# Kernel tuning notes

Hardware: AMD Instinct MI355X
Metric: run time of the kernel (lower is better)

Reference implementation:

```python
import jax, jax.numpy as jnp
import numpy as np
from jax import lax

KERNEL_SIZE = 5
BOUNDARY_WIDTH = 10


def setup_inputs() -> dict:
    key = jax.random.key(0)
    x_in = jax.random.normal(key, (4, 16, 720, 1440), dtype=jnp.float32)
    return {"x_in": x_in}


def _box_sum(a, k):
    """Sum over a k x k window on the last two dims, zero-padded (SAME).
    Zero padding + mask-count division reproduces the clipped-window average."""
    window = (1,) * (a.ndim - 2) + (k, k)
    strides = (1,) * a.ndim
    return lax.reduce_window(a, jnp.array(0, a.dtype), lax.add, window, strides, "SAME")


def reference(x_in) -> jnp.ndarray:
    k = KERNEL_SIZE
    bw = BOUNDARY_WIDTH
    H, W = x_in.shape[-2], x_in.shape[-1]

    ii = jnp.arange(H)
    jj = jnp.arange(W)
    # boundary mask [H, W]: True within boundary_width of any edge
    mb = (((ii < bw) | (ii >= H - bw))[:, None]
          | ((jj < bw) | (jj >= W - bw))[None, :])
    mb_f = mb.astype(x_in.dtype)
    mi_f = 1.0 - mb_f

    # windowed sums of same-class neighbors (zero padding = clipped window)
    num_b = _box_sum(x_in * mb_f, k)   # contributions from boundary pixels
    num_i = _box_sum(x_in * mi_f, k)   # contributions from interior pixels
    cnt_b = _box_sum(mb_f, k)          # [H, W] counts, broadcast over leading dims
    cnt_i = _box_sum(mi_f, k)

    num = jnp.where(mb, num_b, num_i)
    cnt = jnp.where(mb, cnt_b, cnt_i)  # >= 1 wherever selected (pixel counts itself)
    return num / cnt
```

## Files before the change

kernel.cpp:

```cpp
#include <hip/hip_runtime.h>


#define HH 720
#define WW 1440
#define PLANE (HH * WW)
#define NPLANES 64


#define NG 354
#define NCHUNK 29
#define CHUNK 24

__device__ __forceinline__ float4 hsum5(const float* __restrict__ p) {
    const float2 l = *(const float2*)(p - 2);
    const float4 m = *(const float4*)(p);
    const float2 r = *(const float2*)(p + 4);
    float4 h;
    h.x = l.x + l.y + m.x + m.y + m.z;
    h.y = h.x - l.x + m.w;
    h.z = h.y - l.y + r.x;
    h.w = h.z - m.x + r.y;
    return h;
}

__global__ __launch_bounds__(256) void fast_kernel(const float* __restrict__ x,
                                                   float* __restrict__ out) {
    const int id = blockIdx.x * 256 + threadIdx.x;
    if (id >= NG * NCHUNK) return;
    const int chunk = id / NG;
    const int g     = id - chunk * NG;
    const int j0    = 12 + 4 * g;
    const int row0  = 12 + chunk * CHUNK;

    const float* __restrict__ xp = x + (size_t)blockIdx.y * PLANE;
    float* __restrict__ op       = out + (size_t)blockIdx.y * PLANE;

    float4 h[5];
#pragma unroll
    for (int t = 0; t < 4; ++t) {
        h[t] = hsum5(xp + (row0 - 2 + t) * WW + j0);
    }

#pragma unroll
    for (int t = 0; t < CHUNK; ++t) {
        const int r = row0 + t;
        h[(t + 4) % 5] = hsum5(xp + (r + 2) * WW + j0);
        float4 v;
        v.x = ((h[0].x + h[1].x) + (h[2].x + h[3].x)) + h[4].x;
        v.y = ((h[0].y + h[1].y) + (h[2].y + h[3].y)) + h[4].y;
        v.z = ((h[0].z + h[1].z) + (h[2].z + h[3].z)) + h[4].z;
        v.w = ((h[0].w + h[1].w) + (h[2].w + h[3].w)) + h[4].w;
        const float s = 1.0f / 25.0f;
        v.x *= s; v.y *= s; v.z *= s; v.w *= s;
        *(float4*)(op + r * WW + j0) = v;
    }
}


#define NEDGE 51264

__global__ __launch_bounds__(256) void edge_kernel(const float* __restrict__ x,
                                                   float* __restrict__ out) {
    const int p = blockIdx.x * 256 + threadIdx.x;
    if (p >= NEDGE) return;
    int i, j;
    if (p < 34560) {
        i = p / 1440;
        j = p - i * 1440;
        if (i >= 12) i += 696;
    } else {
        const int q  = p - 34560;
        const int qi = q / 24;
        const int r  = q - qi * 24;
        i = 12 + qi;
        j = (r < 12) ? r : r + 1416;
    }

    const float* __restrict__ xp = x + (size_t)blockIdx.y * PLANE;
    const bool cb = (i < 10) | (i >= 710) | (j < 10) | (j >= 1430);

    float s = 0.0f, cnt = 0.0f;
#pragma unroll
    for (int di = -2; di <= 2; ++di) {
#pragma unroll
        for (int dj = -2; dj <= 2; ++dj) {
            const int ni = i + di, nj = j + dj;
            const bool inb = ((unsigned)ni < (unsigned)HH) & ((unsigned)nj < (unsigned)WW);
            const bool nb  = (ni < 10) | (ni >= 710) | (nj < 10) | (nj >= 1430);
            const int ci = min(max(ni, 0), HH - 1);
            const int cj = min(max(nj, 0), WW - 1);
            const float v = xp[ci * WW + cj];
            const float w = (inb && (nb == cb)) ? 1.0f : 0.0f;
            s += w * v;
            cnt += w;
        }
    }
    out[(size_t)blockIdx.y * PLANE + i * WW + j] = s / cnt;
}

extern "C" void kernel_launch(void* const* d_in, const int* in_sizes, int n_in,
                              void* d_out, int out_size, void* d_ws, size_t ws_size,
                              hipStream_t stream) {
    const float* x = (const float*)d_in[0];
    float* out = (float*)d_out;

    dim3 gf((NG * NCHUNK + 255) / 256, NPLANES);
    hipLaunchKernelGGL(fast_kernel, gf, dim3(256), 0, stream, x, out);

    dim3 ge((NEDGE + 255) / 256, NPLANES);
    hipLaunchKernelGGL(edge_kernel, ge, dim3(256), 0, stream, x, out);
}
```

Measured before the change: 469.3 us.

## Prefetch next row in rotating-register stencil loop and shrink row chunks

Splits each row's load from its horizontal sum so the next row's raw values are loaded one iteration ahead of use. The fully unrolled 24-row loop becomes a non-unrolled loop over a five-row register rotation, which cuts code size and register pressure. Chunks drop from 24 to 20 rows with more chunks, giving more threads. A bounds guard skips rows past 707, at the cost of some redundant work and an added branch in the last chunk.

```diff
diff --git a/kernel.cpp b/kernel.cpp
--- a/kernel.cpp
+++ b/kernel.cpp
@@ -6,21 +6,42 @@
 #define PLANE (HH * WW)
 #define NPLANES 64
 
+#define NG 354
+#define CHUNK 20
+#define NCHUNK 35
 
-#define NG 354
-#define NCHUNK 29
-#define CHUNK 24
+struct Raw { float2 l; float4 m; float2 r; };
 
-__device__ __forceinline__ float4 hsum5(const float* __restrict__ p) {
-    const float2 l = *(const float2*)(p - 2);
-    const float4 m = *(const float4*)(p);
-    const float2 r = *(const float2*)(p + 4);
+__device__ __forceinline__ Raw load_row(const float* __restrict__ p) {
+    Raw o;
+    o.l = *(const float2*)(p - 2);
+    o.m = *(const float4*)(p);
+    o.r = *(const float2*)(p + 4);
+    return o;
+}
+
+__device__ __forceinline__ float4 combine(const Raw& w) {
     float4 h;
-    h.x = l.x + l.y + m.x + m.y + m.z;
-    h.y = h.x - l.x + m.w;
-    h.z = h.y - l.y + r.x;
-    h.w = h.z - m.x + r.y;
+    h.x = w.l.x + w.l.y + w.m.x + w.m.y + w.m.z;
+    h.y = h.x - w.l.x + w.m.w;
+    h.z = h.y - w.l.y + w.r.x;
+    h.w = h.z - w.m.x + w.r.y;
     return h;
+}
+
+__device__ __forceinline__ void emit(const float4& a, const float4& b,
+                                     const float4& c, const float4& d,
+                                     const float4& e, float* __restrict__ q,
+                                     int r) {
+    if (r < 708) {
+        const float s = 1.0f / 25.0f;
+        float4 v;
+        v.x = (((a.x + b.x) + (c.x + d.x)) + e.x) * s;
+        v.y = (((a.y + b.y) + (c.y + d.y)) + e.y) * s;
+        v.z = (((a.z + b.z) + (c.z + d.z)) + e.z) * s;
+        v.w = (((a.w + b.w) + (c.w + d.w)) + e.w) * s;
+        *(float4*)q = v;
+    }
 }
 
 __global__ __launch_bounds__(256) void fast_kernel(const float* __restrict__ x,
@@ -35,24 +56,29 @@
     const float* __restrict__ xp = x + (size_t)blockIdx.y * PLANE;
     float* __restrict__ op       = out + (size_t)blockIdx.y * PLANE;
 
-    float4 h[5];
-#pragma unroll
-    for (int t = 0; t < 4; ++t) {
-        h[t] = hsum5(xp + (row0 - 2 + t) * WW + j0);
-    }
+    const float* p = xp + (row0 - 2) * WW + j0;
+    float4 h0 = combine(load_row(p)); p += WW;
+    float4 h1 = combine(load_row(p)); p += WW;
+    float4 h2 = combine(load_row(p)); p += WW;
+    float4 h3 = combine(load_row(p)); p += WW;
+    float4 h4;
+    Raw pre = load_row(p); p += WW;
 
-#pragma unroll
-    for (int t = 0; t < CHUNK; ++t) {
-        const int r = row0 + t;
-        h[(t + 4) % 5] = hsum5(xp + (r + 2) * WW + j0);
-        float4 v;
-        v.x = ((h[0].x + h[1].x) + (h[2].x + h[3].x)) + h[4].x;
-        v.y = ((h[0].y + h[1].y) + (h[2].y + h[3].y)) + h[4].y;
-        v.z = ((h[0].z + h[1].z) + (h[2].z + h[3].z)) + h[4].z;
-        v.w = ((h[0].w + h[1].w) + (h[2].w + h[3].w)) + h[4].w;
-        const float s = 1.0f / 25.0f;
-        v.x *= s; v.y *= s; v.z *= s; v.w *= s;
-        *(float4*)(op + r * WW + j0) = v;
+    float* q = op + row0 * WW + j0;
+    int r = row0;
+
+#pragma unroll 1
+    for (int tb = 0; tb < 4; ++tb) {
+        h4 = combine(pre); pre = load_row(p); p += WW;
+        emit(h0, h1, h2, h3, h4, q, r); q += WW; ++r;
+        h0 = combine(pre); pre = load_row(p); p += WW;
+        emit(h1, h2, h3, h4, h0, q, r); q += WW; ++r;
+        h1 = combine(pre); pre = load_row(p); p += WW;
+        emit(h2, h3, h4, h0, h1, q, r); q += WW; ++r;
+        h2 = combine(pre); pre = load_row(p); p += WW;
+        emit(h3, h4, h0, h1, h2, q, r); q += WW; ++r;
+        h3 = combine(pre); pre = load_row(p); p += WW;
+        emit(h4, h0, h1, h2, h3, q, r); q += WW; ++r;
     }
 }
 
@@ -71,9 +97,9 @@
     } else {
         const int q  = p - 34560;
         const int qi = q / 24;
-        const int r  = q - qi * 24;
+        const int rr = q - qi * 24;
         i = 12 + qi;
-        j = (r < 12) ? r : r + 1416;
+        j = (rr < 12) ? rr : rr + 1416;
     }
 
     const float* __restrict__ xp = x + (size_t)blockIdx.y * PLANE;
```

Result: no change. 473.0 us (+0.8%).
